# Optimization experiments

Measured on AMD Instinct MI355X. Metric: run time of the kernel, lower is better.

## Reference

```python
import jax, jax.numpy as jnp
import numpy as np

B, C, H, W = 2, 64, 192, 192
C8 = C // 8


def setup_inputs() -> dict:
    key = jax.random.key(0)
    ks = jax.random.split(key, 8)
    return {
        "x": jax.random.normal(ks[0], (B, C, H, W), jnp.float32),
        "Wq": jax.random.normal(ks[1], (C8, C), jnp.float32) * 0.05,
        "bq": jax.random.normal(ks[2], (C8,), jnp.float32) * 0.05,
        "Wk": jax.random.normal(ks[3], (C8, C), jnp.float32) * 0.05,
        "bk": jax.random.normal(ks[4], (C8,), jnp.float32) * 0.05,
        "Wv": jax.random.normal(ks[5], (C, C), jnp.float32) * 0.05,
        "bv": jax.random.normal(ks[6], (C,), jnp.float32) * 0.05,
        "gamma": jax.random.normal(ks[7], (1,), jnp.float32),
    }


def _offsets(t):
    # [B, Cc, H, W] -> [B, 16, Cc, L]; per chessboard offset (i,j) in the 4x4
    # block, value = max(t[.., 4h+i, 4w+j], 0)  (mask-then-maxpool in the original)
    b, cc, h, w = t.shape
    hq, wq = h // 4, w // 4
    r = t.reshape(b, cc, hq, 4, wq, 4)
    r = jnp.transpose(r, (0, 3, 5, 1, 2, 4)).reshape(b, 16, cc, hq * wq)
    return jnp.maximum(r, 0.0)


def reference(x, Wq, bq, Wk, bk, Wv, bv, gamma):
    b, c, h, w = x.shape
    hq, wq = h // 4, w // 4
    q = jnp.einsum('oc,bchw->bohw', Wq, x) + bq[None, :, None, None]
    k = jnp.einsum('oc,bchw->bohw', Wk, x) + bk[None, :, None, None]
    v = jnp.einsum('oc,bchw->bohw', Wv, x) + bv[None, :, None, None]
    qs = _offsets(q)  # [B,16,C8,L]
    ks = _offsets(k)  # [B,16,C8,L]
    vs = _offsets(v)  # [B,16,C,L]
    # attn[b,n,l,m] = softmax_m( q_l . k_m )
    attn = jax.nn.softmax(jnp.einsum('bncl,bncm->bnlm', qs, ks), axis=-1)
    out = jnp.einsum('bncm,bnlm->bncl', vs, attn)  # [B,16,C,L]
    # scatter each offset's [C,Hq,Wq] result back to its chessboard position
    out = out.reshape(b, 4, 4, c, hq, wq)
    out = jnp.transpose(out, (0, 3, 4, 1, 5, 2)).reshape(b, c, h, w)
    return gamma[0] * out + x
```

## Files before the change

kernel.cpp:

```cpp
#include <hip/hip_runtime.h>

#define LOG2E 1.44269504088896340736f

constexpr int C_ = 64, H_ = 192, W_ = 192;
constexpr int WQ_ = 48, L_ = 2304;
constexpr int KVB = 64;
constexpr int NMT = L_ / KVB;
constexpr int QROWS = 32;
constexpr int NQT = L_ / QROWS;
constexpr int NBLK = 32 * NQT;
constexpr int NCOL = 18432;
constexpr int PBLK = (NCOL / 64) * 4;

typedef _Float16 half8  __attribute__((ext_vector_type(8)));
typedef short    bf16x8 __attribute__((ext_vector_type(8)));
typedef float    f32x16 __attribute__((ext_vector_type(16)));
typedef uint     u32x2  __attribute__((ext_vector_type(2)));
typedef uint     u32x4  __attribute__((ext_vector_type(4)));

static __device__ inline f32x16 fzero16() {
    f32x16 v;
    #pragma unroll
    for (int i = 0; i < 16; ++i) v[i] = 0.f;
    return v;
}

static __device__ inline uint cvtpk_bf16(float lo, float hi) {
    uint r;
    asm("v_cvt_pk_bf16_f32 %0, %1, %2" : "=v"(r) : "v"(lo), "v"(hi));
    return r;
}

static __device__ inline ushort f2bf(float f) {
    uint u = __builtin_bit_cast(uint, f);
    u = (u + 0x7FFFu + ((u >> 16) & 1u)) >> 16;
    return (ushort)u;
}

__global__ __launch_bounds__(64) void proj_kernel(
    const float* __restrict__ x,
    const float* __restrict__ Wq, const float* __restrict__ bq,
    const float* __restrict__ Wk, const float* __restrict__ bk,
    const float* __restrict__ Wv, const float* __restrict__ bv,
    _Float16* __restrict__ qh, _Float16* __restrict__ kh,
    ushort* __restrict__ vws)
{
    const int bid0 = blockIdx.x;
    const int bid = (bid0 & 7) * (PBLK / 8) + (bid0 >> 3);
    const int cg = bid >> 2;
    const int j  = bid & 3;
    const int lane = threadIdx.x;
    const int C = cg * 64 + lane;
    const int b = C / 9216;
    const int cp = C - b * 9216;
    const int h = cp / 48;
    const int wq = cp - h * 48;
    const int n = (h & 3) * 4 + j;
    const int l = (h >> 2) * 48 + wq;
    const int bn = b * 16 + n;

    const float* xp = x + (size_t)b * 64 * 36864 + cp * 4 + j;

    float acc[20] = {};
    if (j < 3) {
        const float* wbase = Wv + j * 20 * 64;
        #pragma unroll 4
        for (int c = 0; c < 64; ++c) {
            const float xv = xp[(size_t)c * 36864];
            #pragma unroll
            for (int o = 0; o < 20; ++o)
                acc[o] += wbase[o * 64 + c] * xv;
        }
    } else {
        #pragma unroll 4
        for (int c = 0; c < 64; ++c) {
            const float xv = xp[(size_t)c * 36864];
            #pragma unroll
            for (int o = 0; o < 4; ++o)
                acc[o] += Wv[(60 + o) * 64 + c] * xv;
            #pragma unroll
            for (int o = 0; o < 8; ++o)
                acc[4 + o] += Wq[o * 64 + c] * xv;
            #pragma unroll
            for (int o = 0; o < 8; ++o)
                acc[12 + o] += Wk[o * 64 + c] * xv;
        }
    }

    const int mt = l >> 6;
    const int ks4 = (l >> 4) & 3;
    const int m16 = l & 15;
    ushort* vd = vws + (((size_t)bn * NMT + mt) * 4 + ks4) * 1024 + m16;

    if (j < 3) {
        #pragma unroll
        for (int o = 0; o < 20; ++o)
            vd[(20 * j + o) * 16] = f2bf(fmaxf(acc[o] + bv[20 * j + o], 0.f));
    } else {
        #pragma unroll
        for (int o = 0; o < 4; ++o)
            vd[(60 + o) * 16] = f2bf(fmaxf(acc[o] + bv[60 + o], 0.f));
        half8 qv, kv;
        #pragma unroll
        for (int o = 0; o < 8; ++o) {
            qv[o] = (_Float16)(fmaxf((acc[4 + o] + bq[o]) * LOG2E, 0.f));
            kv[o] = (_Float16)fmaxf(acc[12 + o] + bk[o], 0.f);
        }
        *(half8*)(qh + ((size_t)bn * L_ + l) * 8) = qv;
        *(half8*)(kh + ((size_t)bn * L_ + l) * 8) = kv;
    }
}

__global__ __launch_bounds__(256) void attn_kernel(
    const _Float16* __restrict__ qh, const _Float16* __restrict__ kh,
    const ushort* __restrict__ vws, const float* __restrict__ x,
    const float* __restrict__ gamma_p, float* __restrict__ out)
{
    __shared__ float red[4][64][17];
    float* lds_o = &red[0][0][0];

    const int tid = threadIdx.x;
    const int wid = tid >> 6;
    const int lane = tid & 63;
    const int r32 = lane & 31;
    const int hi = lane >> 5;

    const int bid0 = blockIdx.x;
    const int xg = bid0 & 7;
    const int s  = bid0 >> 3;
    const int j4 = s & 3;
    const int lt = s >> 2;
    const int b  = xg >> 2;
    const int n  = (xg & 3) * 4 + j4;
    const int bn = b * 16 + n;
    const int qrow0 = lt * QROWS;

    const _Float16* qb = qh + (size_t)bn * L_ * 8;
    const _Float16* kb = kh + (size_t)bn * L_ * 8;
    const ushort* vaddr = vws + (size_t)bn * NMT * 4096 + r32 * 16 + hi * 8;

    half8 qfrag;
    #pragma unroll
    for (int i = 0; i < 8; ++i) qfrag[i] = (_Float16)0.f;
    if (hi == 0) qfrag = *(const half8*)(qb + (qrow0 + r32) * 8);

    f32x16 acc0 = fzero16(), acc1 = fzero16();
    float psum = 0.f;

    half8 kf0n, kf1n;
    #pragma unroll
    for (int i = 0; i < 8; ++i) { kf0n[i] = (_Float16)0.f; kf1n[i] = (_Float16)0.f; }

    if (hi == 0) {
        kf0n = *(const half8*)(kb + (wid * 64 + r32) * 8);
        kf1n = *(const half8*)(kb + (wid * 64 + 32 + r32) * 8);
    }
    f32x16 s0 = __builtin_amdgcn_mfma_f32_32x32x16_f16(kf0n, qfrag, fzero16(), 0, 0, 0);
    f32x16 s1 = __builtin_amdgcn_mfma_f32_32x32x16_f16(kf1n, qfrag, fzero16(), 0, 0, 0);

    bf16x8 vb0[4], vb1[4];
    vb0[0] = *(const bf16x8*)(vaddr + wid * 4096);
    vb1[0] = *(const bf16x8*)(vaddr + wid * 4096 + 512);
    vb0[1] = *(const bf16x8*)(vaddr + wid * 4096 + 1024);
    vb1[1] = *(const bf16x8*)(vaddr + wid * 4096 + 1024 + 512);
    vb0[2] = *(const bf16x8*)(vaddr + wid * 4096 + 2048);
    vb1[2] = *(const bf16x8*)(vaddr + wid * 4096 + 2048 + 512);

    #pragma unroll 1
    for (int t = 0; t < NMT / 4; ++t) {
        const int mt  = 4 * t + wid;
        const int mtn = (t < NMT / 4 - 1) ? mt + 4 : mt;

        if (hi == 0) {
            kf0n = *(const half8*)(kb + (mtn * 64 + r32) * 8);
            kf1n = *(const half8*)(kb + (mtn * 64 + 32 + r32) * 8);
        }

        #define STAGE(KS, SV, HALF, LS, LOFF)                                  \
        {                                                                      \
            const bf16x8 nv0 = *(const bf16x8*)(vaddr + (LOFF));               \
            const bf16x8 nv1 = *(const bf16x8*)(vaddr + (LOFF) + 512);         \
            float e[8];                                                        \
            _Pragma("unroll")                                                  \
            for (int i = 0; i < 8; ++i)                                        \
                e[i] = __builtin_amdgcn_exp2f(SV[(HALF) * 8 + i]);             \
            psum += ((e[0] + e[1]) + (e[2] + e[3]))                            \
                  + ((e[4] + e[5]) + (e[6] + e[7]));                           \
            const uint pb0 = cvtpk_bf16(e[0], e[1]);                           \
            const uint pb1 = cvtpk_bf16(e[2], e[3]);                           \
            const uint pa0 = cvtpk_bf16(e[4], e[5]);                           \
            const uint pa1 = cvtpk_bf16(e[6], e[7]);                           \
            const u32x2 q0 = __builtin_amdgcn_permlane32_swap(pa0, pb0, false, false); \
            const u32x2 q1 = __builtin_amdgcn_permlane32_swap(pa1, pb1, false, false); \
            u32x4 tt;                                                          \
            tt[0] = q0.y; tt[1] = q1.y; tt[2] = q0.x; tt[3] = q1.x;            \
            const bf16x8 pa = __builtin_bit_cast(bf16x8, tt);                  \
            __builtin_amdgcn_s_setprio(1);                                     \
            acc0 = __builtin_amdgcn_mfma_f32_32x32x16_bf16(pa, vb0[KS], acc0, 0, 0, 0); \
            acc1 = __builtin_amdgcn_mfma_f32_32x32x16_bf16(pa, vb1[KS], acc1, 0, 0, 0); \
            __builtin_amdgcn_s_setprio(0);                                     \
            vb0[LS] = nv0; vb1[LS] = nv1;                                      \
        }

        STAGE(0, s0, 0, 3, mt * 4096 + 3072)
        STAGE(1, s0, 1, 0, mtn * 4096)
        s0 = __builtin_amdgcn_mfma_f32_32x32x16_f16(kf0n, qfrag, fzero16(), 0, 0, 0);
        STAGE(2, s1, 0, 1, mtn * 4096 + 1024)
        STAGE(3, s1, 1, 2, mtn * 4096 + 2048)
        s1 = __builtin_amdgcn_mfma_f32_32x32x16_f16(kf1n, qfrag, fzero16(), 0, 0, 0);
        #undef STAGE
    }

    const uint pu = __builtin_bit_cast(uint, psum);
    const u32x2 pc = __builtin_amdgcn_permlane32_swap(pu, pu, false, false);
    const float other = __builtin_bit_cast(float, (hi == 0) ? pc.x : pc.y);
    const float wsum = psum + other;

    {
        float* dst = &red[wid][lane][0];
        #pragma unroll
        for (int r = 0; r < 16; ++r) dst[r] = acc0[r];
        dst[16] = wsum;
    }
    __syncthreads();

    float rtot = 0.f;
    #pragma unroll
    for (int w4 = 0; w4 < 4; ++w4) rtot += red[w4][lane][16];
    const float rinv = 1.0f / rtot;

    const int sw = wid & 1;
    float fin[8];
    if (wid < 2) {
        #pragma unroll
        for (int i = 0; i < 8; ++i)
            fin[i] = red[0][lane][8 * sw + i] + red[1][lane][8 * sw + i]
                   + red[2][lane][8 * sw + i] + red[3][lane][8 * sw + i];
    }
    __syncthreads();

    {
        float* dst = &red[wid][lane][0];
        #pragma unroll
        for (int r = 0; r < 16; ++r) dst[r] = acc1[r];
    }
    __syncthreads();

    if (wid >= 2) {
        #pragma unroll
        for (int i = 0; i < 8; ++i)
            fin[i] = red[0][lane][8 * sw + i] + red[1][lane][8 * sw + i]
                   + red[2][lane][8 * sw + i] + red[3][lane][8 * sw + i];
    }
    __syncthreads();

    {
        const int chw = r32 + ((wid >= 2) ? 32 : 0);
        #pragma unroll
        for (int i = 0; i < 8; ++i) {
            const int r = 8 * sw + i;
            const int Rg = (r & 3) + 8 * (r >> 2) + 4 * hi;
            const float ri = __shfl(rinv, Rg, 64);
            lds_o[chw * 33 + Rg] = fin[i] * ri;
        }
    }
    __syncthreads();

    const int gl = lane & 31;
    const int ch2 = lane >> 5;
    const int glf = qrow0 + gl;
    const int hh = (glf / WQ_) * 4 + (n >> 2);
    const int ww = (glf % WQ_) * 4 + (n & 3);
    const float g = gamma_p[0];
    const size_t base = ((size_t)b * C_ * H_ + hh) * W_ + ww;
    #pragma unroll
    for (int io = 0; io < 8; ++io) {
        const int ch = io * 8 + wid * 2 + ch2;
        const size_t o = base + (size_t)ch * (H_ * W_);
        out[o] = g * lds_o[ch * 33 + gl] + x[o];
    }
}

extern "C" void kernel_launch(void* const* d_in, const int* in_sizes, int n_in,
                              void* d_out, int out_size, void* d_ws, size_t ws_size,
                              hipStream_t stream) {
    const float* x  = (const float*)d_in[0];
    const float* Wq = (const float*)d_in[1];
    const float* bq = (const float*)d_in[2];
    const float* Wk = (const float*)d_in[3];
    const float* bk = (const float*)d_in[4];
    const float* Wv = (const float*)d_in[5];
    const float* bv = (const float*)d_in[6];
    const float* gamma = (const float*)d_in[7];
    float* out = (float*)d_out;

    _Float16* qh = (_Float16*)d_ws;
    _Float16* kh = qh + (size_t)32 * L_ * 8;
    ushort*   vb = (ushort*)(kh + (size_t)32 * L_ * 8);

    proj_kernel<<<dim3(PBLK), dim3(64), 0, stream>>>(
        x, Wq, bq, Wk, bk, Wv, bv, qh, kh, vb);
    attn_kernel<<<dim3(NBLK), dim3(256), 0, stream>>>(qh, kh, vb, x, gamma, out);
}
```

Baseline: 63.58 us.

## Split attention KV loop across two waves instead of four per block

Attention blocks now use 128 threads (2 waves). Each wave walks half of the key/value tiles instead of a quarter, so per-wave serial work doubles. The cross-wave reduction becomes a single LDS exchange in which each wave keeps one accumulator half and adds its partner's, which cuts the number of syncthreads and halves the LDS buffer. The intent is to lower reduction and sync overhead and to allow more blocks per CU, at the cost of longer per-wave loops and less parallelism inside each block.

```diff
diff --git a/kernel.cpp b/kernel.cpp
--- a/kernel.cpp
+++ b/kernel.cpp
@@ -111,12 +111,12 @@
     }
 }
 
-__global__ __launch_bounds__(256) void attn_kernel(
+__global__ __launch_bounds__(128) void attn_kernel(
     const _Float16* __restrict__ qh, const _Float16* __restrict__ kh,
     const ushort* __restrict__ vws, const float* __restrict__ x,
     const float* __restrict__ gamma_p, float* __restrict__ out)
 {
-    __shared__ float red[4][64][17];
+    __shared__ float red[2][64][17];
     float* lds_o = &red[0][0][0];
 
     const int tid = threadIdx.x;
@@ -167,9 +167,9 @@
     vb1[2] = *(const bf16x8*)(vaddr + wid * 4096 + 2048 + 512);
 
     #pragma unroll 1
-    for (int t = 0; t < NMT / 4; ++t) {
-        const int mt  = 4 * t + wid;
-        const int mtn = (t < NMT / 4 - 1) ? mt + 4 : mt;
+    for (int t = 0; t < NMT / 2; ++t) {
+        const int mt  = 2 * t + wid;
+        const int mtn = (t < NMT / 2 - 1) ? mt + 2 : mt;
 
         if (hi == 0) {
             kf0n = *(const half8*)(kb + (mtn * 64 + r32) * 8);
@@ -218,50 +218,31 @@
 
     {
         float* dst = &red[wid][lane][0];
-        #pragma unroll
-        for (int r = 0; r < 16; ++r) dst[r] = acc0[r];
+        const f32x16& ex = (wid == 0) ? acc1 : acc0;
+        #pragma unroll
+        for (int r = 0; r < 16; ++r) dst[r] = ex[r];
         dst[16] = wsum;
     }
     __syncthreads();
 
-    float rtot = 0.f;
-    #pragma unroll
-    for (int w4 = 0; w4 < 4; ++w4) rtot += red[w4][lane][16];
-    const float rinv = 1.0f / rtot;
-
-    const int sw = wid & 1;
-    float fin[8];
-    if (wid < 2) {
-        #pragma unroll
-        for (int i = 0; i < 8; ++i)
-            fin[i] = red[0][lane][8 * sw + i] + red[1][lane][8 * sw + i]
-                   + red[2][lane][8 * sw + i] + red[3][lane][8 * sw + i];
+    const float* src = &red[wid ^ 1][lane][0];
+    const float rinv = 1.0f / (wsum + src[16]);
+
+    float fin[16];
+    {
+        const f32x16& keep = (wid == 0) ? acc0 : acc1;
+        #pragma unroll
+        for (int r = 0; r < 16; ++r) fin[r] = keep[r] + src[r];
     }
     __syncthreads();
 
     {
-        float* dst = &red[wid][lane][0];
-        #pragma unroll
-        for (int r = 0; r < 16; ++r) dst[r] = acc1[r];
-    }
-    __syncthreads();
-
-    if (wid >= 2) {
-        #pragma unroll
-        for (int i = 0; i < 8; ++i)
-            fin[i] = red[0][lane][8 * sw + i] + red[1][lane][8 * sw + i]
-                   + red[2][lane][8 * sw + i] + red[3][lane][8 * sw + i];
-    }
-    __syncthreads();
-
-    {
-        const int chw = r32 + ((wid >= 2) ? 32 : 0);
-        #pragma unroll
-        for (int i = 0; i < 8; ++i) {
-            const int r = 8 * sw + i;
+        const int chw = r32 + wid * 32;
+        #pragma unroll
+        for (int r = 0; r < 16; ++r) {
             const int Rg = (r & 3) + 8 * (r >> 2) + 4 * hi;
             const float ri = __shfl(rinv, Rg, 64);
-            lds_o[chw * 33 + Rg] = fin[i] * ri;
+            lds_o[chw * 33 + Rg] = fin[r] * ri;
         }
     }
     __syncthreads();
@@ -274,8 +255,8 @@
     const float g = gamma_p[0];
     const size_t base = ((size_t)b * C_ * H_ + hh) * W_ + ww;
     #pragma unroll
-    for (int io = 0; io < 8; ++io) {
-        const int ch = io * 8 + wid * 2 + ch2;
+    for (int io = 0; io < 16; ++io) {
+        const int ch = io * 4 + wid * 2 + ch2;
         const size_t o = base + (size_t)ch * (H_ * W_);
         out[o] = g * lds_o[ch * 33 + gl] + x[o];
     }
@@ -300,5 +281,5 @@
 
     proj_kernel<<<dim3(PBLK), dim3(64), 0, stream>>>(
         x, Wq, bq, Wk, bk, Wv, bv, qh, kh, vb);
-    attn_kernel<<<dim3(NBLK), dim3(256), 0, stream>>>(qh, kh, vb, x, gamma, out);
-}
+    attn_kernel<<<dim3(NBLK), dim3(128), 0, stream>>>(qh, kh, vb, x, gamma, out);
+}
```

Result: no change. 63.74 us (+0.3%).
